# Performance work log

Measured on AMD Instinct MI355X. Metric: run time of the kernel, lower is better.

Reference implementation:

```python
import jax, jax.numpy as jnp
import numpy as np


def decode_e4m3(bits):
    """Decode raw FP8 E4M3 byte patterns (int32 in [0,256)) to float32.

    Layout: 1 sign bit, 4 exponent bits (bias 7), 3 mantissa bits.
    exp==0 -> subnormal: mant/8 * 2^-6. The NaN pattern (exp==15, man==7)
    is remapped to the max normal magnitude 448 to keep the reference
    NaN-free for randomized inputs.
    """
    b = bits.astype(jnp.int32)
    sign = jnp.where((b & 0x80) != 0, -1.0, 1.0).astype(jnp.float32)
    exp = (b >> 3) & 0xF
    man = (b & 0x7).astype(jnp.float32)
    # remap NaN encoding (exp=15, man=7) to max normal 448 = (1+6/8)*2^8
    man = jnp.where((exp == 15) & (man == 7.0), 6.0, man)
    sub = man * jnp.float32(2.0 ** -9)                     # man/8 * 2^-6
    norm = (1.0 + man / 8.0) * jnp.exp2((exp - 7).astype(jnp.float32))
    return sign * jnp.where(exp == 0, sub, norm)


def setup_inputs() -> dict:
    key = jax.random.key(0)
    k1, k2, k3, k4 = jax.random.split(key, 4)
    T, D_IN, D_OUT = 8192, 4096, 8192  # tokens (2x4096), in_features, out_features
    x = jax.random.normal(k1, (T, D_IN), dtype=jnp.float32)
    weight_fp8 = jax.random.randint(k2, (D_OUT, D_IN), 0, 256, dtype=jnp.int32)
    weight_scales = jax.random.uniform(k3, (D_OUT,), dtype=jnp.float32)
    bias = jax.random.normal(k4, (D_OUT,), dtype=jnp.float32)
    return {"x": x, "weight_fp8": weight_fp8, "weight_scales": weight_scales, "bias": bias}


def reference(x, weight_fp8, weight_scales, bias):
    # Fused FP8 dequant + GEMM + bias: W = decode(w_fp8) * scale[:, None]
    w = decode_e4m3(weight_fp8) * weight_scales[:, None]   # [out, in]
    return jnp.einsum("ti,oi->to", x, w) + bias[None, :]
```

## Files before the change

### kernel.cpp

```cpp
#include <hip/hip_runtime.h>

using short8 = __attribute__((ext_vector_type(8))) short;
using bf16x8 = __attribute__((ext_vector_type(8))) __bf16;
using f32x4  = __attribute__((ext_vector_type(4))) float;

__device__ __forceinline__ void gload_lds16(const void* g, void* l) {
  __builtin_amdgcn_global_load_lds(
      (const __attribute__((address_space(1))) void*)g,
      (__attribute__((address_space(3))) void*)l, 16, 0, 0);
}


__device__ __forceinline__ float dec_e4m3(int b) {
  int e = (b >> 3) & 15;
  int m = b & 7;
  if (e == 15 && m == 7) m = 6;
  float v;
  if (e) v = (1.0f + (float)m * 0.125f) * __uint_as_float((unsigned)(e + 120) << 23);
  else   v = (float)m * 0.001953125f;
  return (b & 0x80) ? -v : v;
}

__global__ void dec_w_kernel(const int* __restrict__ wq,
                             unsigned short* __restrict__ wb, int n8) {
  int i = blockIdx.x * blockDim.x + threadIdx.x;
  if (i >= n8) return;
  const int4* p = (const int4*)wq + (size_t)i * 2;
  int4 a = p[0], b4 = p[1];
  int bv[8] = {a.x, a.y, a.z, a.w, b4.x, b4.y, b4.z, b4.w};
  short8 r;
#pragma unroll
  for (int j = 0; j < 8; ++j) {
    float f = dec_e4m3(bv[j]);
    r[j] = (short)(__float_as_uint(f) >> 16);
  }
  *(short8*)(wb + (size_t)i * 8) = r;
}

__global__ void cvt_x_kernel(const float* __restrict__ x,
                             unsigned short* __restrict__ xb, int n8) {
  int i = blockIdx.x * blockDim.x + threadIdx.x;
  if (i >= n8) return;
  const float4* p = (const float4*)x + (size_t)i * 2;
  float4 a = p[0], b4 = p[1];
  float v[8] = {a.x, a.y, a.z, a.w, b4.x, b4.y, b4.z, b4.w};
  short8 r;
#pragma unroll
  for (int j = 0; j < 8; ++j) {
    unsigned u = __float_as_uint(v[j]);
    u += 0x7FFFu + ((u >> 16) & 1u);
    r[j] = (short)(u >> 16);
  }
  *(short8*)(xb + (size_t)i * 8) = r;
}


#define NOPV ((void)0)
#define VM6 asm volatile("s_waitcnt vmcnt(6)" ::: "memory")
#define VM0 asm volatile("s_waitcnt vmcnt(0)" ::: "memory")

#define STAGE_A(GP, LBUF, KT, J) do { \
    const char* _g = (GP) + (size_t)(KT) * 128u; \
    gload_lds16(_g + (size_t)((J) * 64) * Kb, (LBUF) + ((J) * 64) * 128 + tdA); \
    gload_lds16(_g + (size_t)(128 + (J) * 64) * Kb, (LBUF) + (128 + (J) * 64) * 128 + tdA); \
  } while (0)

#define STAGE_B(GP, LBUF, KT, J) do { \
    const char* _g = (GP) + (size_t)(KT) * 128u; \
    gload_lds16(_g + (size_t)((J) * 32) * Kb, (LBUF) + ((J) * 32) * 128 + tdB); \
    gload_lds16(_g + (size_t)(128 + (J) * 32) * Kb, (LBUF) + (128 + (J) * 32) * 128 + tdB); \
  } while (0)

#define RD_A(DST, LB, QM) do { \
    _Pragma("unroll") \
    for (int mi = 0; mi < 4; ++mi) { \
      const char* _b = lds + (LB) + (size_t)(arow + (QM) * 64 + mi * 16) * 128; \
      (DST)[mi * 2 + 0] = *(const bf16x8*)(_b + fo0); \
      (DST)[mi * 2 + 1] = *(const bf16x8*)(_b + fo1); \
    } \
  } while (0)

#define RD_B(DST, LB, QN) do { \
    _Pragma("unroll") \
    for (int ni = 0; ni < 2; ++ni) { \
      const char* _b = lds + (LB) + 32768 + (size_t)(brow + ((QN) * 2 + ni) * 16) * 128; \
      (DST)[ni * 2 + 0] = *(const bf16x8*)(_b + fo0); \
      (DST)[ni * 2 + 1] = *(const bf16x8*)(_b + fo1); \
    } \
  } while (0)

#define PH(AB, BB, QM, QN, STBLK, VMBLK, PFBLK) do { \
    __builtin_amdgcn_s_setprio(1); \
    _Pragma("unroll") \
    for (int mi = 0; mi < 4; ++mi) \
      _Pragma("unroll") \
      for (int ni = 0; ni < 2; ++ni) \
        _Pragma("unroll") \
        for (int ks = 0; ks < 2; ++ks) \
          acc[(QM) * 4 + mi][(QN) * 2 + ni] = __builtin_amdgcn_mfma_f32_16x16x32_bf16( \
              (AB)[mi * 2 + ks], (BB)[ni * 2 + ks], acc[(QM) * 4 + mi][(QN) * 2 + ni], 0, 0, 0); \
    __builtin_amdgcn_s_setprio(0); \
    __builtin_amdgcn_sched_barrier(0); \
    STBLK; \
    VMBLK; \
    PFBLK; \
    __builtin_amdgcn_s_barrier(); \
  } while (0)

__global__ __launch_bounds__(512, 2) void gemm256_kernel(
    const unsigned short* __restrict__ A, const unsigned short* __restrict__ B,
    const float* __restrict__ scale, const float* __restrict__ bias,
    float* __restrict__ out, int T, int K, int N) {
  extern __shared__ char lds[];
  char* const lA0 = lds;
  char* const lB0 = lds + 32768;
  char* const lA1 = lds + 65536;
  char* const lB1 = lds + 98304;
  const int L0A = 0, L0B = 0, L1A = 65536, L1B = 65536;

  const int nbn = N >> 8;
  const int nbm = T >> 8;
  int bm, bn, CH;
  if (((nbm & 3) == 0) && ((nbn & 7) == 0) &&
      (int)gridDim.x == (nbm >> 2) * nbn) {
    const int xcd = blockIdx.x & 7, off = blockIdx.x >> 3;
    const int cpx = nbn >> 3;
    const int col = xcd * cpx + (off % cpx);
    const int ci  = off / cpx;
    bm = (ci * 4) << 8;
    bn = col << 8;
    CH = 4;
  } else {
    const int nwg = nbm * nbn;
    const int q = nwg >> 3, r = nwg & 7;
    const int xcd = blockIdx.x & 7, off = blockIdx.x >> 3;
    const int swz = (xcd < r ? xcd * (q + 1) : r * (q + 1) + (xcd - r) * q) + off;
    bm = (swz / nbn) << 8;
    bn = (swz % nbn) << 8;
    CH = 1;
  }

  const int tid = threadIdx.x;
  const int wave = tid >> 6, lane = tid & 63;
  const int wm = wave >> 2, wn = wave & 3;
  const int nt = K >> 6;
  const size_t Kb = (size_t)K * 2;

  const int trow = tid >> 3;
  const int gcol = ((tid & 7) * 16) ^ (((tid >> 3) & 7) << 4);
  const int bmap = ((tid & 256) ? 64 : 0) + ((tid >> 6) & 3) * 8 + ((tid >> 3) & 7);
  const char* gAb = (const char*)A + (size_t)(bm + trow) * Kb + gcol;
  const char* gBb = (const char*)B + (size_t)(bn + bmap) * Kb + gcol;
  const int tdA = tid * 16;
  const int tdB = bmap * 128 + (tid & 7) * 16;

  const int g16 = lane >> 4, l8 = lane & 7;
  const int fo0 = ((g16 ^ l8) << 4);
  const int fo1 = fo0 ^ 64;
  const int arow = wm * 128 + (lane & 15);
  const int brow = wn * 64 + (lane & 15);

  const int ccol = bn + wn * 64 + (lane & 15);
  int crow = bm + wm * 128 + ((lane >> 4) << 2);
  float scv[4], biv[4];
#pragma unroll
  for (int ni = 0; ni < 4; ++ni) {
    scv[ni] = scale[ccol + ni * 16];
    biv[ni] = bias[ccol + ni * 16];
  }

  f32x4 acc[8][4] = {};
  bf16x8 aE[8], aO[8], b0a[4], b0b[4], b1[4];

  for (int ch = 0; ch < CH; ++ch) {
    const bool more = (ch + 1 < CH);
    const char* gAn = gAb + (size_t)256 * Kb;

    if (ch == 0) {
      STAGE_A(gAb, lA0, 0, 0);
      STAGE_B(gBb, lB0, 0, 0);
      STAGE_B(gBb, lB0, 0, 1);
      STAGE_A(gAb, lA0, 0, 1);
      STAGE_A(gAb, lA1, 1, 0);
      STAGE_B(gBb, lB1, 1, 0);
      STAGE_B(gBb, lB1, 1, 1);
      VM6;
      __builtin_amdgcn_s_barrier();
      RD_A(aE, L0A, 0);
      RD_B(b0a, L0B, 0);
    }

    int t = 0;
    for (; t + 3 < nt; t += 2) {
      PH(aE, b0a, 0, 0, STAGE_A(gAb, lA1, t + 1, 1), NOPV, RD_B(b1, L0B, 1));
      PH(aE, b1,  0, 1, STAGE_A(gAb, lA0, t + 2, 0), NOPV, RD_A(aO, L0A, 1));
      PH(aO, b1,  1, 1, STAGE_B(gBb, lB0, t + 2, 0), NOPV, NOPV);
      PH(aO, b0a, 1, 0, STAGE_B(gBb, lB0, t + 2, 1), VM6,
         { RD_A(aE, L1A, 0); RD_B(b0b, L1B, 0); });
      PH(aE, b0b, 0, 0, STAGE_A(gAb, lA0, t + 2, 1), NOPV, RD_B(b1, L1B, 1));
      PH(aE, b1,  0, 1, STAGE_A(gAb, lA1, t + 3, 0), NOPV, RD_A(aO, L1A, 1));
      PH(aO, b1,  1, 1, STAGE_B(gBb, lB1, t + 3, 0), NOPV, NOPV);
      PH(aO, b0b, 1, 0, STAGE_B(gBb, lB1, t + 3, 1), VM6,
         { RD_A(aE, L0A, 0); RD_B(b0a, L0B, 0); });
    }
    PH(aE, b0a, 0, 0, STAGE_A(gAb, lA1, t + 1, 1), NOPV, RD_B(b1, L0B, 1));
    PH(aE, b1,  0, 1, NOPV, NOPV, RD_A(aO, L0A, 1));
    PH(aO, b1,  1, 1, NOPV, NOPV, NOPV);
    PH(aO, b0a, 1, 0, NOPV, VM0, { RD_A(aE, L1A, 0); RD_B(b0b, L1B, 0); });
    PH(aE, b0b, 0, 0, { if (more) STAGE_A(gAn, lA0, 0, 0); }, NOPV, RD_B(b1, L1B, 1));
    PH(aE, b1,  0, 1, { if (more) STAGE_B(gBb, lB0, 0, 0); }, NOPV, RD_A(aO, L1A, 1));
    PH(aO, b1,  1, 1, { if (more) STAGE_B(gBb, lB0, 0, 1); }, NOPV, NOPV);
    PH(aO, b0b, 1, 0, { if (more) STAGE_A(gAn, lA0, 0, 1); }, NOPV, NOPV);

#pragma unroll
    for (int ni = 0; ni < 4; ++ni) {
      const int o = ccol + ni * 16;
#pragma unroll
      for (int mi = 0; mi < 8; ++mi) {
#pragma unroll
        for (int rr = 0; rr < 4; ++rr) {
          __builtin_nontemporal_store(acc[mi][ni][rr] * scv[ni] + biv[ni],
                                      &out[(size_t)(crow + mi * 16 + rr) * N + o]);
        }
      }
    }

    if (more) {
#pragma unroll
      for (int mi = 0; mi < 8; ++mi)
#pragma unroll
        for (int ni = 0; ni < 4; ++ni)
          acc[mi][ni] = (f32x4){0.f, 0.f, 0.f, 0.f};
      STAGE_A(gAn, lA1, 1, 0);
      STAGE_B(gBb, lB1, 1, 0);
      STAGE_B(gBb, lB1, 1, 1);
      VM6;
      __builtin_amdgcn_s_barrier();
      RD_A(aE, L0A, 0);
      RD_B(b0a, L0B, 0);
      gAb = gAn;
      crow += 256;
    }
  }
}


#define BM 128
#define BN 128
#define BK 64

__global__ __launch_bounds__(256) void gemm_bf16_kernel(
    const unsigned short* __restrict__ A, const unsigned short* __restrict__ B,
    const float* __restrict__ scale, const float* __restrict__ bias,
    float* __restrict__ out, int T, int K, int N) {
  __shared__ __align__(16) unsigned short lsA[BM * BK];
  __shared__ __align__(16) unsigned short lsB[BN * BK];

  const int nbn = N / BN;
  const int nwg = (T / BM) * nbn;
  const int q = nwg >> 3, r = nwg & 7;
  const int xcd = blockIdx.x & 7, off = blockIdx.x >> 3;
  const int swz = (xcd < r ? xcd * (q + 1) : r * (q + 1) + (xcd - r) * q) + off;
  const int bm = (swz / nbn) * BM;
  const int bn = (swz % nbn) * BN;

  const int tid = threadIdx.x;
  const int wave = tid >> 6, lane = tid & 63;
  const int wm = (wave >> 1) * 64, wn = (wave & 1) * 64;

  f32x4 acc[4][4] = {};

  const int srow = (wave << 3) + (lane >> 3);
  const int scolb = (lane & 7) * 16;
  const size_t Kb = (size_t)K * 2;
  const char* gA = (const char*)A + (size_t)bm * Kb + scolb;
  const char* gB = (const char*)B + (size_t)bn * Kb + scolb;
  char* laddrA = (char*)lsA + wave * 1024;
  char* laddrB = (char*)lsB + wave * 1024;

  for (int k0 = 0; k0 < K; k0 += BK) {
    const char* pa = gA + (size_t)k0 * 2;
    const char* pb = gB + (size_t)k0 * 2;
#pragma unroll
    for (int s = 0; s < 4; ++s) {
      int row = s * 32 + srow;
      gload_lds16(pa + (size_t)row * Kb, laddrA + s * 4096);
      gload_lds16(pb + (size_t)row * Kb, laddrB + s * 4096);
    }
    __syncthreads();

    const int arow2 = wm + (lane & 15);
    const int brow2 = wn + (lane & 15);
#pragma unroll
    for (int kk = 0; kk < BK; kk += 32) {
      const int kcol = kk + ((lane >> 4) << 3);
      bf16x8 af[4], bfr[4];
#pragma unroll
      for (int i = 0; i < 4; ++i)
        af[i] = *(const bf16x8*)(lsA + (size_t)(arow2 + i * 16) * BK + kcol);
#pragma unroll
      for (int i = 0; i < 4; ++i)
        bfr[i] = *(const bf16x8*)(lsB + (size_t)(brow2 + i * 16) * BK + kcol);
#pragma unroll
      for (int mi = 0; mi < 4; ++mi)
#pragma unroll
        for (int ni = 0; ni < 4; ++ni)
          acc[mi][ni] = __builtin_amdgcn_mfma_f32_16x16x32_bf16(
              af[mi], bfr[ni], acc[mi][ni], 0, 0, 0);
    }
    __syncthreads();
  }

  const int ccol = bn + wn + (lane & 15);
  const int crow0 = bm + wm + ((lane >> 4) << 2);
#pragma unroll
  for (int ni = 0; ni < 4; ++ni) {
    const int o = ccol + ni * 16;
    const float sc = scale[o], bi = bias[o];
#pragma unroll
    for (int mi = 0; mi < 4; ++mi) {
#pragma unroll
      for (int rr = 0; rr < 4; ++rr) {
        const int t2 = crow0 + mi * 16 + rr;
        out[(size_t)t2 * N + o] = acc[mi][ni][rr] * sc + bi;
      }
    }
  }
}


__global__ void naive_kernel(const float* __restrict__ X, const int* __restrict__ Wq,
                             const float* __restrict__ sc, const float* __restrict__ bs,
                             float* __restrict__ out, int T, int K, int N) {
  __shared__ float xt[16][16];
  __shared__ float wt[16][17];
  const int tx = threadIdx.x & 15, ty = threadIdx.x >> 4;
  const int t = blockIdx.y * 16 + ty, o = blockIdx.x * 16 + tx;
  float acc = 0.f;
  for (int k0 = 0; k0 < K; k0 += 16) {
    xt[ty][tx] = X[(size_t)t * K + k0 + tx];
    wt[ty][tx] = dec_e4m3(Wq[(size_t)(blockIdx.x * 16 + ty) * K + k0 + tx]);
    __syncthreads();
#pragma unroll
    for (int kk = 0; kk < 16; ++kk) acc += xt[ty][kk] * wt[tx][kk];
    __syncthreads();
  }
  out[(size_t)t * N + o] = acc * sc[o] + bs[o];
}

extern "C" void kernel_launch(void* const* d_in, const int* in_sizes, int n_in,
                              void* d_out, int out_size, void* d_ws, size_t ws_size,
                              hipStream_t stream) {
  const float* x  = (const float*)d_in[0];
  const int*   wq = (const int*)d_in[1];
  const float* sc = (const float*)d_in[2];
  const float* bi = (const float*)d_in[3];
  float* out = (float*)d_out;

  const int DOUT = in_sizes[2];
  const int DIN  = in_sizes[1] / DOUT;
  const int T    = in_sizes[0] / DIN;

  const size_t need = ((size_t)T * DIN + (size_t)DOUT * DIN) * 2;
  const bool ok256 = (T % 256 == 0) && (DOUT % 256 == 0) && (DIN % 256 == 0);
  const bool ok128 = (T % BM == 0) && (DOUT % BN == 0) && (DIN % BK == 0);

  if (ws_size >= need && (ok256 || ok128)) {
    unsigned short* xb = (unsigned short*)d_ws;
    unsigned short* wb = xb + (size_t)T * DIN;
    const int nx8 = (int)((size_t)T * DIN / 8);
    const int nw8 = (int)((size_t)DOUT * DIN / 8);
    cvt_x_kernel<<<(nx8 + 255) / 256, 256, 0, stream>>>(x, xb, nx8);
    dec_w_kernel<<<(nw8 + 255) / 256, 256, 0, stream>>>(wq, wb, nw8);
    if (ok256) {
      const int nbm = T >> 8, nbn = DOUT >> 8;
      const bool okchain = ((nbm & 3) == 0) && ((nbn & 7) == 0);
      const int grid = okchain ? (nbm >> 2) * nbn : nbm * nbn;
      gemm256_kernel<<<grid, 512, 131072, stream>>>(xb, wb, sc, bi, out, T, DIN, DOUT);
    } else {
      dim3 grid((T / BM) * (DOUT / BN));
      gemm_bf16_kernel<<<grid, 256, 0, stream>>>(xb, wb, sc, bi, out, T, DIN, DOUT);
    }
  } else {
    dim3 g(DOUT / 16, T / 16);
    naive_kernel<<<g, 256, 0, stream>>>(x, wq, sc, bi, out, T, DIN, DOUT);
  }
}
```

Measured before the change: 515.8 us.

## Merge MFMA phases pairwise to halve barriers in the 256-tile pipeline

Restructures the 8-phase software pipeline of the 256x256 GEMM into 4 double-size phases, each issuing 32 MFMAs, two staging loads and a larger LDS prefetch before one barrier. Separate b1a/b1b register buffers replace the single b1 so both B quarter-tiles are loaded at once. The aim is fewer s_barrier synchronisations and less phase overhead per K step. The cost is more live VGPRs and coarser interleaving of loads with MFMA, which could hurt latency hiding or occupancy at 2 waves/SIMD.

Measured after the change: 555.7 us. 7.7% more time.

```diff
diff --git a/kernel.cpp b/kernel.cpp
--- a/kernel.cpp
+++ b/kernel.cpp
@@ -89,8 +89,7 @@
     } \
   } while (0)
 
-#define PH(AB, BB, QM, QN, STBLK, VMBLK, PFBLK) do { \
-    __builtin_amdgcn_s_setprio(1); \
+#define MF16(AB, BB, QM, QN) \
     _Pragma("unroll") \
     for (int mi = 0; mi < 4; ++mi) \
       _Pragma("unroll") \
@@ -98,7 +97,12 @@
         _Pragma("unroll") \
         for (int ks = 0; ks < 2; ++ks) \
           acc[(QM) * 4 + mi][(QN) * 2 + ni] = __builtin_amdgcn_mfma_f32_16x16x32_bf16( \
-              (AB)[mi * 2 + ks], (BB)[ni * 2 + ks], acc[(QM) * 4 + mi][(QN) * 2 + ni], 0, 0, 0); \
+              (AB)[mi * 2 + ks], (BB)[ni * 2 + ks], acc[(QM) * 4 + mi][(QN) * 2 + ni], 0, 0, 0);
+
+#define PH2(AB1, BB1, QM1, QN1, AB2, BB2, QM2, QN2, STBLK, VMBLK, PFBLK) do { \
+    __builtin_amdgcn_s_setprio(1); \
+    MF16(AB1, BB1, QM1, QN1) \
+    MF16(AB2, BB2, QM2, QN2) \
     __builtin_amdgcn_s_setprio(0); \
     __builtin_amdgcn_sched_barrier(0); \
     STBLK; \
@@ -170,7 +174,7 @@
   }
 
   f32x4 acc[8][4] = {};
-  bf16x8 aE[8], aO[8], b0a[4], b0b[4], b1[4];
+  bf16x8 aE[8], aO[8], b0a[4], b0b[4], b1a[4], b1b[4];
 
   for (int ch = 0; ch < CH; ++ch) {
     const bool more = (ch + 1 < CH);
@@ -188,29 +192,34 @@
       __builtin_amdgcn_s_barrier();
       RD_A(aE, L0A, 0);
       RD_B(b0a, L0B, 0);
+      RD_B(b1a, L0B, 1);
     }
 
     int t = 0;
     for (; t + 3 < nt; t += 2) {
-      PH(aE, b0a, 0, 0, STAGE_A(gAb, lA1, t + 1, 1), NOPV, RD_B(b1, L0B, 1));
-      PH(aE, b1,  0, 1, STAGE_A(gAb, lA0, t + 2, 0), NOPV, RD_A(aO, L0A, 1));
-      PH(aO, b1,  1, 1, STAGE_B(gBb, lB0, t + 2, 0), NOPV, NOPV);
-      PH(aO, b0a, 1, 0, STAGE_B(gBb, lB0, t + 2, 1), VM6,
-         { RD_A(aE, L1A, 0); RD_B(b0b, L1B, 0); });
-      PH(aE, b0b, 0, 0, STAGE_A(gAb, lA0, t + 2, 1), NOPV, RD_B(b1, L1B, 1));
-      PH(aE, b1,  0, 1, STAGE_A(gAb, lA1, t + 3, 0), NOPV, RD_A(aO, L1A, 1));
-      PH(aO, b1,  1, 1, STAGE_B(gBb, lB1, t + 3, 0), NOPV, NOPV);
-      PH(aO, b0b, 1, 0, STAGE_B(gBb, lB1, t + 3, 1), VM6,
-         { RD_A(aE, L0A, 0); RD_B(b0a, L0B, 0); });
-    }
-    PH(aE, b0a, 0, 0, STAGE_A(gAb, lA1, t + 1, 1), NOPV, RD_B(b1, L0B, 1));
-    PH(aE, b1,  0, 1, NOPV, NOPV, RD_A(aO, L0A, 1));
-    PH(aO, b1,  1, 1, NOPV, NOPV, NOPV);
-    PH(aO, b0a, 1, 0, NOPV, VM0, { RD_A(aE, L1A, 0); RD_B(b0b, L1B, 0); });
-    PH(aE, b0b, 0, 0, { if (more) STAGE_A(gAn, lA0, 0, 0); }, NOPV, RD_B(b1, L1B, 1));
-    PH(aE, b1,  0, 1, { if (more) STAGE_B(gBb, lB0, 0, 0); }, NOPV, RD_A(aO, L1A, 1));
-    PH(aO, b1,  1, 1, { if (more) STAGE_B(gBb, lB0, 0, 1); }, NOPV, NOPV);
-    PH(aO, b0b, 1, 0, { if (more) STAGE_A(gAn, lA0, 0, 1); }, NOPV, NOPV);
+      PH2(aE, b0a, 0, 0, aE, b1a, 0, 1,
+          { STAGE_A(gAb, lA1, t + 1, 1); STAGE_A(gAb, lA0, t + 2, 0); },
+          NOPV, RD_A(aO, L0A, 1));
+      PH2(aO, b1a, 1, 1, aO, b0a, 1, 0,
+          { STAGE_B(gBb, lB0, t + 2, 0); STAGE_B(gBb, lB0, t + 2, 1); },
+          VM6, { RD_A(aE, L1A, 0); RD_B(b0b, L1B, 0); RD_B(b1b, L1B, 1); });
+      PH2(aE, b0b, 0, 0, aE, b1b, 0, 1,
+          { STAGE_A(gAb, lA0, t + 2, 1); STAGE_A(gAb, lA1, t + 3, 0); },
+          NOPV, RD_A(aO, L1A, 1));
+      PH2(aO, b1b, 1, 1, aO, b0b, 1, 0,
+          { STAGE_B(gBb, lB1, t + 3, 0); STAGE_B(gBb, lB1, t + 3, 1); },
+          VM6, { RD_A(aE, L0A, 0); RD_B(b0a, L0B, 0); RD_B(b1a, L0B, 1); });
+    }
+    PH2(aE, b0a, 0, 0, aE, b1a, 0, 1,
+        STAGE_A(gAb, lA1, t + 1, 1), NOPV, RD_A(aO, L0A, 1));
+    PH2(aO, b1a, 1, 1, aO, b0a, 1, 0,
+        NOPV, VM0, { RD_A(aE, L1A, 0); RD_B(b0b, L1B, 0); RD_B(b1b, L1B, 1); });
+    PH2(aE, b0b, 0, 0, aE, b1b, 0, 1,
+        { if (more) { STAGE_A(gAn, lA0, 0, 0); STAGE_B(gBb, lB0, 0, 0); } },
+        NOPV, RD_A(aO, L1A, 1));
+    PH2(aO, b1b, 1, 1, aO, b0b, 1, 0,
+        { if (more) { STAGE_B(gBb, lB0, 0, 1); STAGE_A(gAn, lA0, 0, 1); } },
+        NOPV, NOPV);
 
 #pragma unroll
     for (int ni = 0; ni < 4; ++ni) {
@@ -238,6 +247,7 @@
       __builtin_amdgcn_s_barrier();
       RD_A(aE, L0A, 0);
       RD_B(b0a, L0B, 0);
+      RD_B(b1a, L0B, 1);
       gAb = gAn;
       crow += 256;
     }
```
